# Kernel tuning notes

Hardware: AMD Instinct MI355X
Metric: run time of the kernel (lower is better)

## Reference

```python
import jax, jax.numpy as jnp
import numpy as np

B, T, DM = 2, 512, 1024
H, DH = 16, 64          # n_heads, d_head = d_model // n_heads
D, R = 32, 4            # d_manifold, metric_net rank
TEMP_MIN = 0.5


def _rope_tables(t_len, d_head):
    inv_freq = 1.0 / (10000.0 ** (jnp.arange(0, d_head, 2, dtype=jnp.float32) / d_head))
    t = jnp.arange(t_len, dtype=jnp.float32)
    freqs = t[:, None] * inv_freq[None, :]          # [T, d_head//2]
    emb = jnp.concatenate([freqs, freqs], axis=-1)  # [T, d_head]
    return jnp.cos(emb), jnp.sin(emb)


def _apply_rope(x, cos, sin):
    # x: [B, H, T, d_head]
    half = x.shape[-1] // 2
    x1, x2 = x[..., :half], x[..., half:]
    c1 = cos[None, None, :, :half]
    s1 = sin[None, None, :, :half]
    return jnp.concatenate([x1 * c1 - x2 * s1, x1 * s1 + x2 * c1], axis=-1)


def setup_inputs() -> dict:
    key = jax.random.key(0)
    ks = jax.random.split(key, 9)
    s = 0.02
    return {
        "x": jax.random.normal(ks[0], (B, T, DM), dtype=jnp.float32),
        "Wq": s * jax.random.normal(ks[1], (DM, DM), dtype=jnp.float32),
        "Wk": s * jax.random.normal(ks[2], (DM, DM), dtype=jnp.float32),
        "Wv": s * jax.random.normal(ks[3], (DM, DM), dtype=jnp.float32),
        "Wo": s * jax.random.normal(ks[4], (DM, DM), dtype=jnp.float32),
        "Wqm": s * jax.random.normal(ks[5], (DH, D), dtype=jnp.float32),
        "Wkm": s * jax.random.normal(ks[6], (DH, D), dtype=jnp.float32),
        "Wmetric": s * jax.random.normal(ks[7], (D, D * R), dtype=jnp.float32),
        "temperature": jnp.asarray(1.0, dtype=jnp.float32),
    }


def reference(x, Wq, Wk, Wv, Wo, Wqm, Wkm, Wmetric, temperature):
    b, t, c = x.shape
    # projections -> [B, H, T, d_head]
    def split_heads(y):
        return y.reshape(b, t, H, DH).transpose(0, 2, 1, 3)
    q = split_heads(x @ Wq)
    k = split_heads(x @ Wk)
    v = split_heads(x @ Wv)

    cos, sin = _rope_tables(t, DH)
    q = _apply_rope(q, cos, sin)
    k = _apply_rope(k, cos, sin)

    # manifold coordinates in (0,1): [B, H, T, D]
    qm = jax.nn.sigmoid(jnp.einsum('bhtd,dm->bhtm', q, Wqm))
    km = jax.nn.sigmoid(jnp.einsum('bhtd,dm->bhtm', k, Wkm))

    # low-rank metric factor U(q): [B, H, T, D, R]
    U = jnp.einsum('bhtm,mn->bhtn', qm, Wmetric).reshape(b, H, t, D, R)

    # Euclidean part: ||q_i - k_j||^2 = |q|^2 + |k|^2 - 2 q.k  -> [B,H,T,T]
    q2 = jnp.sum(qm * qm, axis=-1)
    k2 = jnp.sum(km * km, axis=-1)
    qk = jnp.einsum('bhid,bhjd->bhij', qm, km)
    dist_euc = q2[..., :, None] + k2[..., None, :] - 2.0 * qk

    # low-rank part: ||U_i^T (q_i - k_j)||^2, factorized as U_i^T q_i - U_i^T k_j
    Uq = jnp.einsum('bhidr,bhid->bhir', U, qm)          # [B,H,T,R]
    Uk = jnp.einsum('bhidr,bhjd->bhijr', U, km)         # [B,H,T,T,R]
    dist_lr = jnp.sum((Uq[:, :, :, None, :] - Uk) ** 2, axis=-1)

    dist_sq = jnp.maximum(dist_euc + dist_lr, 0.0)

    temp = jnp.maximum(temperature, TEMP_MIN)
    attn = -dist_sq / temp

    causal = jnp.triu(jnp.ones((t, t), dtype=bool), k=1)
    attn = jnp.where(causal[None, None], -jnp.inf, attn)
    attn = jax.nn.softmax(attn, axis=-1)

    out = jnp.einsum('bhij,bhjd->bhid', attn, v)        # [B,H,T,d_head]
    out = out.transpose(0, 2, 1, 3).reshape(b, t, c)
    return out @ Wo
```

## Files before the change

### kernel.cpp

```cpp
#include <hip/hip_runtime.h>
#include <cmath>

constexpr int B_  = 2;
constexpr int T_  = 512;
constexpr int DM_ = 1024;
constexpr int H_  = 16;
constexpr int DH_ = 64;
constexpr int D_  = 32;
constexpr int R_  = 4;
constexpr int BH_ = B_ * H_;

typedef __bf16 bf16x8 __attribute__((ext_vector_type(8)));
typedef float  f32x4  __attribute__((ext_vector_type(4)));
typedef unsigned short u16x8 __attribute__((ext_vector_type(8)));

__device__ __forceinline__ unsigned short f2bf(float f) {
    unsigned u = __float_as_uint(f);
    return (unsigned short)((u + 0x7fffu + ((u >> 16) & 1u)) >> 16);
}
__device__ __forceinline__ float bf2f(unsigned short v) {
    return __uint_as_float((unsigned)v << 16);
}
__device__ __forceinline__ void gload16(const void* g, void* l) {
    __builtin_amdgcn_global_load_lds(
        (const __attribute__((address_space(1))) void*)g,
        (__attribute__((address_space(3))) void*)l, 16, 0, 0);
}

__global__ __launch_bounds__(256) void prep_kernel(
    const float* __restrict__ x,
    const float* __restrict__ Wq, const float* __restrict__ Wk,
    const float* __restrict__ Wv, const float* __restrict__ Wo,
    unsigned short* __restrict__ xb,
    unsigned short* __restrict__ wqb, unsigned short* __restrict__ wkb,
    unsigned short* __restrict__ wvb, unsigned short* __restrict__ wob)
{
    const int t = threadIdx.x;
    const int z = blockIdx.z;
    if (z == 4) {
        int base = (blockIdx.y * 16 + blockIdx.x) * 4096 + t * 16;
#pragma unroll
        for (int c = 0; c < 4; ++c) {
            float4 v = *(const float4*)&x[base + c * 4];
            ushort4 o = { f2bf(v.x), f2bf(v.y), f2bf(v.z), f2bf(v.w) };
            *(ushort4*)&xb[base + c * 4] = o;
        }
        return;
    }
    __shared__ __align__(16) unsigned short Ls[64][72];
    const float* W = (z == 0) ? Wq : (z == 1) ? Wk : (z == 2) ? Wv : Wo;
    unsigned short* O = (z == 0) ? wqb : (z == 1) ? wkb : (z == 2) ? wvb : wob;
    const int k0 = blockIdx.x * 64;
    const int n0 = blockIdx.y * 64;
#pragma unroll
    for (int it = 0; it < 4; ++it) {
        int r = it * 16 + (t >> 4);
        int c = (t & 15) * 4;
        float4 v4 = *(const float4*)&W[(size_t)(k0 + r) * DM_ + n0 + c];
        Ls[c + 0][r] = f2bf(v4.x); Ls[c + 1][r] = f2bf(v4.y);
        Ls[c + 2][r] = f2bf(v4.z); Ls[c + 3][r] = f2bf(v4.w);
    }
    __syncthreads();
#pragma unroll
    for (int it = 0; it < 2; ++it) {
        int nl = it * 32 + (t >> 3);
        int kc = (t & 7) * 8;
        *(u16x8*)&O[(size_t)(n0 + nl) * DM_ + k0 + kc] = *(const u16x8*)&Ls[nl][kc];
    }
}

__global__ __launch_bounds__(256) void gemm_qkv(
    const unsigned short* __restrict__ A,
    const unsigned short* __restrict__ Bt0,
    const unsigned short* __restrict__ Bt1,
    const unsigned short* __restrict__ Bt2,
    float* __restrict__ C0, float* __restrict__ C1,
    unsigned short* __restrict__ vT)
{
    __shared__ __align__(16) unsigned short As[2][64 * 64];
    __shared__ __align__(16) unsigned short Bs[2][64 * 64];
    const int tid  = threadIdx.x;
    const int lane = tid & 63;
    const int w    = tid >> 6;
    const int wm   = (w & 1) * 32;
    const int wn   = (w >> 1) * 32;
    const int l15  = lane & 15, quad = lane >> 4;

    const int wg   = (blockIdx.x & 7) * 96 + (blockIdx.x >> 3);
    const int bm   = (wg & 15) * 64;
    const int nidx = wg >> 4;
    const int n0   = nidx * 64;
    const int which = n0 >> 10;
    const int bn   = n0 & 1023;
    const unsigned short* Bt = (which == 0) ? Bt0 : (which == 1) ? Bt1 : Bt2;

    const int srow = tid >> 3, kcs = tid & 7, kcg = kcs ^ (srow & 7);
    const unsigned short* Ap0 = A  + (size_t)(bm + srow) * DM_ + kcg * 8;
    const unsigned short* Bp0 = Bt + (size_t)(bn + srow) * DM_ + kcg * 8;
    const unsigned short* Ap1 = Ap0 + 32 * DM_;
    const unsigned short* Bp1 = Bp0 + 32 * DM_;

    gload16(Ap0, &As[0][tid * 8]);
    gload16(Ap1, &As[0][tid * 8 + 2048]);
    gload16(Bp0, &Bs[0][tid * 8]);
    gload16(Bp1, &Bs[0][tid * 8 + 2048]);

    f32x4 acc[2][2] = {};
#pragma unroll
    for (int k = 0; k < 16; ++k) {
        const int cur = k & 1, nxt = cur ^ 1;
        __builtin_amdgcn_s_barrier();
        if (k + 1 < 16) {
            const int off = (k + 1) * 64;
            gload16(Ap0 + off, &As[nxt][tid * 8]);
            gload16(Ap1 + off, &As[nxt][tid * 8 + 2048]);
            gload16(Bp0 + off, &Bs[nxt][tid * 8]);
            gload16(Bp1 + off, &Bs[nxt][tid * 8 + 2048]);
            __builtin_amdgcn_s_waitcnt(0x0F74);
        } else {
            __builtin_amdgcn_s_waitcnt(0x0F70);
        }
        __builtin_amdgcn_s_barrier();

        bf16x8 af[2][2], bfr[2][2];
#pragma unroll
        for (int ki = 0; ki < 2; ++ki)
#pragma unroll
            for (int i = 0; i < 2; ++i) {
                int ra = wm + i * 16 + l15;
                int rb = wn + i * 16 + l15;
                int kch = ki * 4 + quad;
                af[ki][i]  = *(const bf16x8*)&As[cur][ra * 64 + (kch ^ (ra & 7)) * 8];
                bfr[ki][i] = *(const bf16x8*)&Bs[cur][rb * 64 + (kch ^ (rb & 7)) * 8];
            }
#pragma unroll
        for (int mi = 0; mi < 2; ++mi)
#pragma unroll
            for (int ni = 0; ni < 2; ++ni) {
                acc[mi][ni] = __builtin_amdgcn_mfma_f32_16x16x32_bf16(
                    af[0][mi], bfr[0][ni], acc[mi][ni], 0, 0, 0);
                acc[mi][ni] = __builtin_amdgcn_mfma_f32_16x16x32_bf16(
                    af[1][mi], bfr[1][ni], acc[mi][ni], 0, 0, 0);
            }
    }

#pragma unroll
    for (int mi = 0; mi < 2; ++mi)
#pragma unroll
        for (int ni = 0; ni < 2; ++ni) {
            f32x4 a = acc[mi][ni];
            int col = wn + ni * 16 + l15;
            int h = bn >> 6, d = col;
#pragma unroll
            for (int r = 0; r < 4; ++r) {
                int row = bm + wm + mi * 16 + quad * 4 + r;
                int bb = row >> 9, tt = row & (T_ - 1);
                if (which == 2) {
                    vT[(((size_t)bb * H_ + h) * DH_ + d) * T_ + tt] = f2bf(a[r]);
                } else {
                    float* C = (which == 0) ? C0 : C1;
                    C[(((size_t)bb * H_ + h) * T_ + tt) * DH_ + d] = a[r];
                }
            }
        }
}

__global__ __launch_bounds__(256) void gemm_out(
    const unsigned short* __restrict__ A,
    const unsigned short* __restrict__ Bt,
    float* __restrict__ C0)
{
    __shared__ __align__(16) unsigned short As[2][64 * 64];
    __shared__ __align__(16) unsigned short Bs[2][64 * 64];
    const int tid  = threadIdx.x;
    const int lane = tid & 63;
    const int w    = tid >> 6;
    const int wm   = (w & 1) * 32;
    const int wn   = (w >> 1) * 32;
    const int l15  = lane & 15, quad = lane >> 4;

    const int bm = blockIdx.y * 64;
    const int bn = blockIdx.x * 64;

    const int srow = tid >> 3, kcs = tid & 7, kcg = kcs ^ (srow & 7);
    const unsigned short* Ap0 = A  + (size_t)(bm + srow) * DM_ + kcg * 8;
    const unsigned short* Bp0 = Bt + (size_t)(bn + srow) * DM_ + kcg * 8;
    const unsigned short* Ap1 = Ap0 + 32 * DM_;
    const unsigned short* Bp1 = Bp0 + 32 * DM_;

    gload16(Ap0, &As[0][tid * 8]);
    gload16(Ap1, &As[0][tid * 8 + 2048]);
    gload16(Bp0, &Bs[0][tid * 8]);
    gload16(Bp1, &Bs[0][tid * 8 + 2048]);

    f32x4 acc[2][2] = {};
#pragma unroll
    for (int k = 0; k < 16; ++k) {
        const int cur = k & 1, nxt = cur ^ 1;
        __builtin_amdgcn_s_barrier();
        if (k + 1 < 16) {
            const int off = (k + 1) * 64;
            gload16(Ap0 + off, &As[nxt][tid * 8]);
            gload16(Ap1 + off, &As[nxt][tid * 8 + 2048]);
            gload16(Bp0 + off, &Bs[nxt][tid * 8]);
            gload16(Bp1 + off, &Bs[nxt][tid * 8 + 2048]);
            __builtin_amdgcn_s_waitcnt(0x0F74);
        } else {
            __builtin_amdgcn_s_waitcnt(0x0F70);
        }
        __builtin_amdgcn_s_barrier();

        bf16x8 af[2][2], bfr[2][2];
#pragma unroll
        for (int ki = 0; ki < 2; ++ki)
#pragma unroll
            for (int i = 0; i < 2; ++i) {
                int ra = wm + i * 16 + l15;
                int rb = wn + i * 16 + l15;
                int kch = ki * 4 + quad;
                af[ki][i]  = *(const bf16x8*)&As[cur][ra * 64 + (kch ^ (ra & 7)) * 8];
                bfr[ki][i] = *(const bf16x8*)&Bs[cur][rb * 64 + (kch ^ (rb & 7)) * 8];
            }
#pragma unroll
        for (int mi = 0; mi < 2; ++mi)
#pragma unroll
            for (int ni = 0; ni < 2; ++ni) {
                acc[mi][ni] = __builtin_amdgcn_mfma_f32_16x16x32_bf16(
                    af[0][mi], bfr[0][ni], acc[mi][ni], 0, 0, 0);
                acc[mi][ni] = __builtin_amdgcn_mfma_f32_16x16x32_bf16(
                    af[1][mi], bfr[1][ni], acc[mi][ni], 0, 0, 0);
            }
    }

#pragma unroll
    for (int mi = 0; mi < 2; ++mi)
#pragma unroll
        for (int ni = 0; ni < 2; ++ni) {
            f32x4 a = acc[mi][ni];
            int col = wn + ni * 16 + l15;
#pragma unroll
            for (int r = 0; r < 4; ++r) {
                int row = bm + wm + mi * 16 + quad * 4 + r;
                C0[(size_t)row * DM_ + bn + col] = a[r];
            }
        }
}

__global__ __launch_bounds__(256) void feat_both(
    const float* __restrict__ q_raw, const float* __restrict__ k_raw,
    const float* __restrict__ Wqm,   const float* __restrict__ Wkm,
    const float* __restrict__ Wmetric,
    unsigned short* __restrict__ a_hi, unsigned short* __restrict__ a_lo,
    unsigned short* __restrict__ km_hi, unsigned short* __restrict__ km_lo,
    float* __restrict__ q2p, float* __restrict__ k2,
    unsigned short* __restrict__ Urb)
{
    const bool QSIDE = (blockIdx.y == 0);
    const float* raw = QSIDE ? q_raw : k_raw;
    const float* Wm  = QSIDE ? Wqm   : Wkm;

    __shared__ float qrs[4][64];
    __shared__ float qms[4][32];
    const int tid  = threadIdx.x;
    const int w    = tid >> 6;
    const int lane = tid & 63;
    const int row  = blockIdx.x * 4 + w;
    const int t    = row & (T_ - 1);
    const int bh   = row >> 9;

    const int m  = lane & 31;
    const int hh = lane >> 5;

    float rv = raw[(size_t)row * 64 + lane];
    float ang = (float)t * expf((float)m * -0.28782313662425575f);
    float s, c;
    sincosf(ang, &s, &c);
    float partner = __shfl_xor(rv, 32);
    float qr = (lane < 32) ? (rv * c - partner * s) : (partner * s + rv * c);
    qrs[w][lane] = qr;

    float acc = 0.f;
#pragma unroll 8
    for (int i = 0; i < 32; ++i) {
        int d = hh * 32 + i;
        acc += qrs[w][d] * Wm[d * 32 + m];
    }
    acc += __shfl_xor(acc, 32);
    const float qm = 1.0f / (1.0f + __expf(-acc));
    if (hh == 0) qms[w][m] = qm;

    if (!QSIDE) {
        if (lane < 32) {
            unsigned short hi = f2bf(qm);
            unsigned short lo = f2bf(qm - bf2f(hi));
            size_t off = (size_t)row * 32 + lane;
            km_hi[off] = hi; km_lo[off] = lo;
        }
        float sq = (lane < 32) ? qm * qm : 0.f;
        sq += __shfl_xor(sq, 32); sq += __shfl_xor(sq, 16);
        sq += __shfl_xor(sq, 8);  sq += __shfl_xor(sq, 4);
        sq += __shfl_xor(sq, 2);  sq += __shfl_xor(sq, 1);
        if (lane == 0) k2[row] = sq;
        return;
    }

    float a0 = 0.f, a1 = 0.f;
#pragma unroll 8
    for (int mm = 0; mm < 32; ++mm) {
        float qv = qms[w][mm];
        float2 wv = *(const float2*)&Wmetric[mm * 128 + lane * 2];
        a0 += qv * wv.x;
        a1 += qv * wv.y;
    }

    {
        int n0i = lane * 2;
        int r0 = n0i & 3, d0 = n0i >> 2;
        Urb[(((size_t)bh * R_ + r0    ) * T_ + t) * D_ + d0] = f2bf(a0);
        Urb[(((size_t)bh * R_ + r0 + 1) * T_ + t) * D_ + d0] = f2bf(a1);
    }

    float dq = qms[w][lane >> 1];
    float u0 = a0 * dq, u1 = a1 * dq;
    u0 += __shfl_xor(u0, 2);  u1 += __shfl_xor(u1, 2);
    u0 += __shfl_xor(u0, 4);  u1 += __shfl_xor(u1, 4);
    u0 += __shfl_xor(u0, 8);  u1 += __shfl_xor(u1, 8);
    u0 += __shfl_xor(u0, 16); u1 += __shfl_xor(u1, 16);
    u0 += __shfl_xor(u0, 32); u1 += __shfl_xor(u1, 32);
    float v0 = __shfl_xor(u0, 1), v1 = __shfl_xor(u1, 1);
    const bool odd = (lane & 1);
    float Uq0 = odd ? v0 : u0;
    float Uq1 = odd ? v1 : u1;
    float Uq2 = odd ? u0 : v0;
    float Uq3 = odd ? u1 : v1;

    {
        int src = m * 2;
        float s0 = __shfl(a0, src);
        float s1 = __shfl(a1, src);
        float s2 = __shfl(a0, src + 1);
        float s3 = __shfl(a1, src + 1);
        if (lane < 32) {
            float b = Uq0 * s0 + Uq1 * s1 + Uq2 * s2 + Uq3 * s3;
            float a = qm + b;
            unsigned short hi = f2bf(a);
            unsigned short lo = f2bf(a - bf2f(hi));
            size_t off = (size_t)row * 32 + lane;
            a_hi[off] = hi; a_lo[off] = lo;
        }
    }

    float sq = (lane < 32) ? qm * qm : 0.f;
    sq += __shfl_xor(sq, 32); sq += __shfl_xor(sq, 16);
    sq += __shfl_xor(sq, 8);  sq += __shfl_xor(sq, 4);
    sq += __shfl_xor(sq, 2);  sq += __shfl_xor(sq, 1);
    if (lane == 0)
        q2p[row] = sq + Uq0 * Uq0 + Uq1 * Uq1 + Uq2 * Uq2 + Uq3 * Uq3;
}

constexpr int PROW = 40;
__global__ __launch_bounds__(256) void attn_mfma(
    const unsigned short* __restrict__ a_hi, const unsigned short* __restrict__ a_lo,
    const unsigned short* __restrict__ km_hi, const unsigned short* __restrict__ km_lo,
    const unsigned short* __restrict__ Urb,
    const float* __restrict__ q2p, const float* __restrict__ k2,
    const float* __restrict__ temp_p, const unsigned short* __restrict__ vT,
    unsigned short* __restrict__ ctxb)
{
    __shared__ __align__(16) unsigned short P_lds[4][32 * PROW];
    __shared__ __align__(16) float OP[4][32][64];
    __shared__ float ML[4][32];

    const int itile = blockIdx.x, bh = blockIdx.y;
    const int i0 = itile * 32;
    const int tid = threadIdx.x, w = tid >> 6, lane = tid & 63;
    const int l15 = lane & 15, quad = lane >> 4;

    const float inv_temp = 1.0f / fmaxf(temp_p[0], 0.5f);

    bf16x8 Ahi[2], Alo[2], Aur[4][2];
#pragma unroll
    for (int mi = 0; mi < 2; ++mi) {
        size_t ab = ((size_t)bh * T_ + i0 + mi * 16 + l15) * 32 + quad * 8;
        Ahi[mi] = *(const bf16x8*)&a_hi[ab];
        Alo[mi] = *(const bf16x8*)&a_lo[ab];
#pragma unroll
        for (int r = 0; r < 4; ++r)
            Aur[r][mi] = *(const bf16x8*)
                &Urb[(((size_t)bh * R_ + r) * T_ + i0 + mi * 16 + l15) * 32 + quad * 8];
    }
    float q2r[2][4];
#pragma unroll
    for (int mi = 0; mi < 2; ++mi)
#pragma unroll
        for (int rg = 0; rg < 4; ++rg)
            q2r[mi][rg] = q2p[(size_t)bh * T_ + i0 + mi * 16 + quad * 4 + rg];

    f32x4 Oacc[2][4] = {};
    float psum[2][4] = {};

    for (int jt = w; jt <= itile; jt += 4) {
        const int j0 = jt * 32;
        bf16x8 Bhi[2], Blo[2];
#pragma unroll
        for (int ni = 0; ni < 2; ++ni) {
            size_t kb = ((size_t)bh * T_ + j0 + ni * 16 + l15) * 32 + quad * 8;
            Bhi[ni] = *(const bf16x8*)&km_hi[kb];
            Blo[ni] = *(const bf16x8*)&km_lo[kb];
        }
        f32x4 acc[2][2] = {};
#pragma unroll
        for (int mi = 0; mi < 2; ++mi)
#pragma unroll
            for (int ni = 0; ni < 2; ++ni) {
                acc[mi][ni] = __builtin_amdgcn_mfma_f32_16x16x32_bf16(
                    Alo[mi], Bhi[ni], acc[mi][ni], 0, 0, 0);
                acc[mi][ni] = __builtin_amdgcn_mfma_f32_16x16x32_bf16(
                    Ahi[mi], Blo[ni], acc[mi][ni], 0, 0, 0);
                acc[mi][ni] = __builtin_amdgcn_mfma_f32_16x16x32_bf16(
                    Ahi[mi], Bhi[ni], acc[mi][ni], 0, 0, 0);
            }
        f32x4 sq[2][2] = {};
#pragma unroll
        for (int r = 0; r < 4; ++r) {
            f32x4 ar[2][2] = {};
#pragma unroll
            for (int mi = 0; mi < 2; ++mi)
#pragma unroll
                for (int ni = 0; ni < 2; ++ni)
                    ar[mi][ni] = __builtin_amdgcn_mfma_f32_16x16x32_bf16(
                        Aur[r][mi], Bhi[ni], ar[mi][ni], 0, 0, 0);
#pragma unroll
            for (int mi = 0; mi < 2; ++mi)
#pragma unroll
                for (int ni = 0; ni < 2; ++ni)
                    sq[mi][ni] += ar[mi][ni] * ar[mi][ni];
        }
        float k2c[2];
#pragma unroll
        for (int ni = 0; ni < 2; ++ni)
            k2c[ni] = k2[(size_t)bh * T_ + j0 + ni * 16 + l15];
        const bool diag = (jt == itile);
#pragma unroll
        for (int mi = 0; mi < 2; ++mi)
#pragma unroll
            for (int ni = 0; ni < 2; ++ni)
#pragma unroll
                for (int rg = 0; rg < 4; ++rg) {
                    float dist = q2r[mi][rg] + k2c[ni]
                               - 2.f * acc[mi][ni][rg] + sq[mi][ni][rg];
                    float sc = -fmaxf(dist, 0.f) * inv_temp;
                    if (diag && (ni * 16 + l15) > (mi * 16 + quad * 4 + rg))
                        sc = -1e30f;
                    float p = __expf(sc);
                    psum[mi][rg] += p;
                    P_lds[w][(mi * 16 + quad * 4 + rg) * PROW + ni * 16 + l15] = f2bf(p);
                }
        bf16x8 Pf[2], Vf[4];
#pragma unroll
        for (int mi = 0; mi < 2; ++mi)
            Pf[mi] = *(const bf16x8*)&P_lds[w][(mi * 16 + l15) * PROW + quad * 8];
#pragma unroll
        for (int n4 = 0; n4 < 4; ++n4)
            Vf[n4] = *(const bf16x8*)
                &vT[((size_t)bh * DH_ + n4 * 16 + l15) * T_ + j0 + quad * 8];
#pragma unroll
        for (int mi = 0; mi < 2; ++mi)
#pragma unroll
            for (int n4 = 0; n4 < 4; ++n4)
                Oacc[mi][n4] = __builtin_amdgcn_mfma_f32_16x16x32_bf16(
                    Pf[mi], Vf[n4], Oacc[mi][n4], 0, 0, 0);
    }

#pragma unroll
    for (int mi = 0; mi < 2; ++mi)
#pragma unroll
        for (int rg = 0; rg < 4; ++rg) {
            float v = psum[mi][rg];
            v += __shfl_xor(v, 1); v += __shfl_xor(v, 2);
            v += __shfl_xor(v, 4); v += __shfl_xor(v, 8);
            psum[mi][rg] = v;
        }
    if (l15 == 0)
#pragma unroll
        for (int mi = 0; mi < 2; ++mi)
#pragma unroll
            for (int rg = 0; rg < 4; ++rg)
                ML[w][mi * 16 + quad * 4 + rg] = psum[mi][rg];
#pragma unroll
    for (int mi = 0; mi < 2; ++mi)
#pragma unroll
        for (int n4 = 0; n4 < 4; ++n4)
#pragma unroll
            for (int rg = 0; rg < 4; ++rg)
                OP[w][mi * 16 + quad * 4 + rg][n4 * 16 + l15] = Oacc[mi][n4][rg];
    __syncthreads();

    const int ii = tid >> 3, ds = tid & 7;
    float l = ML[0][ii] + ML[1][ii] + ML[2][ii] + ML[3][ii];
    float O[8] = {};
#pragma unroll
    for (int wv = 0; wv < 4; ++wv) {
        float4 o0 = *(const float4*)&OP[wv][ii][ds * 8];
        float4 o1 = *(const float4*)&OP[wv][ii][ds * 8 + 4];
        O[0] += o0.x; O[1] += o0.y; O[2] += o0.z; O[3] += o0.w;
        O[4] += o1.x; O[5] += o1.y; O[6] += o1.z; O[7] += o1.w;
    }
    const float inv = 1.0f / l;
    const int b = bh >> 4, h = bh & 15;
    u16x8 o;
#pragma unroll
    for (int dd = 0; dd < 8; ++dd) o[dd] = f2bf(O[dd] * inv);
    *(u16x8*)&ctxb[((size_t)b * T_ + i0 + ii) * DM_ + h * 64 + ds * 8] = o;
}

extern "C" void kernel_launch(void* const* d_in, const int* in_sizes, int n_in,
                              void* d_out, int out_size, void* d_ws, size_t ws_size,
                              hipStream_t stream)
{
    const float* x       = (const float*)d_in[0];
    const float* Wq      = (const float*)d_in[1];
    const float* Wk      = (const float*)d_in[2];
    const float* Wv      = (const float*)d_in[3];
    const float* Wo      = (const float*)d_in[4];
    const float* Wqm     = (const float*)d_in[5];
    const float* Wkm     = (const float*)d_in[6];
    const float* Wmetric = (const float*)d_in[7];
    const float* temp    = (const float*)d_in[8];
    float* out = (float*)d_out;
    float* ws  = (float*)d_ws;

    float* q_raw = ws;
    float* k_raw = q_raw + (size_t)BH_ * T_ * DH_;
    float* q2p   = k_raw + (size_t)BH_ * T_ * DH_;
    float* k2    = q2p   + (size_t)BH_ * T_;
    unsigned short* xb   = (unsigned short*)(k2 + (size_t)BH_ * T_);
    unsigned short* wqb  = xb   + (size_t)DM_ * DM_;
    unsigned short* wkb  = wqb  + (size_t)DM_ * DM_;
    unsigned short* wvb  = wkb  + (size_t)DM_ * DM_;
    unsigned short* wob  = wvb  + (size_t)DM_ * DM_;
    unsigned short* a_hi = wob  + (size_t)DM_ * DM_;
    unsigned short* a_lo = a_hi + (size_t)BH_ * T_ * D_;
    unsigned short* kmhi = a_lo + (size_t)BH_ * T_ * D_;
    unsigned short* kmlo = kmhi + (size_t)BH_ * T_ * D_;
    unsigned short* Urb  = kmlo + (size_t)BH_ * T_ * D_;
    unsigned short* vT   = Urb  + (size_t)BH_ * R_ * T_ * D_;
    unsigned short* ctxb = (unsigned short*)q_raw;

    prep_kernel<<<dim3(16, 16, 5), 256, 0, stream>>>(
        x, Wq, Wk, Wv, Wo, xb, wqb, wkb, wvb, wob);
    gemm_qkv<<<dim3(768), 256, 0, stream>>>(
        xb, wqb, wkb, wvb, q_raw, k_raw, vT);
    feat_both<<<dim3(BH_ * T_ / 4, 2), 256, 0, stream>>>(
        q_raw, k_raw, Wqm, Wkm, Wmetric,
        a_hi, a_lo, kmhi, kmlo, q2p, k2, Urb);
    attn_mfma<<<dim3(T_ / 32, BH_), 256, 0, stream>>>(
        a_hi, a_lo, kmhi, kmlo, Urb, q2p, k2, temp, vT, ctxb);
    gemm_out<<<dim3(16, 16), 256, 0, stream>>>(
        ctxb, wob, out);
}
```

Before: 149.5 us.

## Fuse all stages into one persistent kernel with software grid barriers

Replaces the five separate kernel launches (weight/input bf16 conversion, QKV GEMM, feature computation, attention, output GEMM) with one persistent kernel of 512 blocks. The stages run as grid-stride loops separated by an atomic-counter grid barrier, and a memset resets the counter before launch. The goal is to remove launch gaps and tail effects between the small stages. In exchange, every stage gets the same 512-block grid and shared-memory budget, the spin barriers cost time, and correctness depends on all 512 blocks being co-resident.

After: 363.4 us. 143% more time.

```diff
diff --git a/kernel.cpp b/kernel.cpp
--- a/kernel.cpp
+++ b/kernel.cpp
@@ -27,491 +27,489 @@
         (__attribute__((address_space(3))) void*)l, 16, 0, 0);
 }
 
-__global__ __launch_bounds__(256) void prep_kernel(
-    const float* __restrict__ x,
-    const float* __restrict__ Wq, const float* __restrict__ Wk,
-    const float* __restrict__ Wv, const float* __restrict__ Wo,
-    unsigned short* __restrict__ xb,
-    unsigned short* __restrict__ wqb, unsigned short* __restrict__ wkb,
-    unsigned short* __restrict__ wvb, unsigned short* __restrict__ wob)
-{
-    const int t = threadIdx.x;
-    const int z = blockIdx.z;
-    if (z == 4) {
-        int base = (blockIdx.y * 16 + blockIdx.x) * 4096 + t * 16;
-#pragma unroll
-        for (int c = 0; c < 4; ++c) {
-            float4 v = *(const float4*)&x[base + c * 4];
-            ushort4 o = { f2bf(v.x), f2bf(v.y), f2bf(v.z), f2bf(v.w) };
-            *(ushort4*)&xb[base + c * 4] = o;
-        }
-        return;
-    }
-    __shared__ __align__(16) unsigned short Ls[64][72];
-    const float* W = (z == 0) ? Wq : (z == 1) ? Wk : (z == 2) ? Wv : Wo;
-    unsigned short* O = (z == 0) ? wqb : (z == 1) ? wkb : (z == 2) ? wvb : wob;
-    const int k0 = blockIdx.x * 64;
-    const int n0 = blockIdx.y * 64;
-#pragma unroll
-    for (int it = 0; it < 4; ++it) {
-        int r = it * 16 + (t >> 4);
-        int c = (t & 15) * 4;
-        float4 v4 = *(const float4*)&W[(size_t)(k0 + r) * DM_ + n0 + c];
-        Ls[c + 0][r] = f2bf(v4.x); Ls[c + 1][r] = f2bf(v4.y);
-        Ls[c + 2][r] = f2bf(v4.z); Ls[c + 3][r] = f2bf(v4.w);
+constexpr int PROW = 40;
+
+__device__ __forceinline__ void grid_barrier(unsigned* cnt, unsigned target) {
+    __syncthreads();
+    if (threadIdx.x == 0) {
+        __threadfence();
+        atomicAdd(cnt, 1u);
+        while (atomicAdd(cnt, 0u) < target)
+            __builtin_amdgcn_s_sleep(8);
+        __threadfence();
     }
     __syncthreads();
-#pragma unroll
-    for (int it = 0; it < 2; ++it) {
-        int nl = it * 32 + (t >> 3);
-        int kc = (t & 7) * 8;
-        *(u16x8*)&O[(size_t)(n0 + nl) * DM_ + k0 + kc] = *(const u16x8*)&Ls[nl][kc];
-    }
 }
 
-__global__ __launch_bounds__(256) void gemm_qkv(
-    const unsigned short* __restrict__ A,
-    const unsigned short* __restrict__ Bt0,
-    const unsigned short* __restrict__ Bt1,
-    const unsigned short* __restrict__ Bt2,
-    float* __restrict__ C0, float* __restrict__ C1,
-    unsigned short* __restrict__ vT)
+__global__ __launch_bounds__(256, 2) void mega(
+    const float* x, const float* Wq, const float* Wk,
+    const float* Wv, const float* Wo,
+    const float* Wqm, const float* Wkm, const float* Wmetric,
+    const float* temp_p, float* out,
+    unsigned short* xb, unsigned short* wqb, unsigned short* wkb,
+    unsigned short* wvb, unsigned short* wob,
+    float* q_raw, float* k_raw, float* q2p, float* k2,
+    unsigned short* a_hi, unsigned short* a_lo,
+    unsigned short* km_hi, unsigned short* km_lo,
+    unsigned short* Urb, unsigned short* vT, unsigned short* ctxb,
+    unsigned* bar)
 {
-    __shared__ __align__(16) unsigned short As[2][64 * 64];
-    __shared__ __align__(16) unsigned short Bs[2][64 * 64];
+    __shared__ __align__(16) unsigned char smem[45056];
+
     const int tid  = threadIdx.x;
     const int lane = tid & 63;
     const int w    = tid >> 6;
-    const int wm   = (w & 1) * 32;
-    const int wn   = (w >> 1) * 32;
     const int l15  = lane & 15, quad = lane >> 4;
 
-    const int wg   = (blockIdx.x & 7) * 96 + (blockIdx.x >> 3);
-    const int bm   = (wg & 15) * 64;
-    const int nidx = wg >> 4;
-    const int n0   = nidx * 64;
-    const int which = n0 >> 10;
-    const int bn   = n0 & 1023;
-    const unsigned short* Bt = (which == 0) ? Bt0 : (which == 1) ? Bt1 : Bt2;
-
-    const int srow = tid >> 3, kcs = tid & 7, kcg = kcs ^ (srow & 7);
-    const unsigned short* Ap0 = A  + (size_t)(bm + srow) * DM_ + kcg * 8;
-    const unsigned short* Bp0 = Bt + (size_t)(bn + srow) * DM_ + kcg * 8;
-    const unsigned short* Ap1 = Ap0 + 32 * DM_;
-    const unsigned short* Bp1 = Bp0 + 32 * DM_;
-
-    gload16(Ap0, &As[0][tid * 8]);
-    gload16(Ap1, &As[0][tid * 8 + 2048]);
-    gload16(Bp0, &Bs[0][tid * 8]);
-    gload16(Bp1, &Bs[0][tid * 8 + 2048]);
-
-    f32x4 acc[2][2] = {};
-#pragma unroll
-    for (int k = 0; k < 16; ++k) {
-        const int cur = k & 1, nxt = cur ^ 1;
-        __builtin_amdgcn_s_barrier();
-        if (k + 1 < 16) {
-            const int off = (k + 1) * 64;
-            gload16(Ap0 + off, &As[nxt][tid * 8]);
-            gload16(Ap1 + off, &As[nxt][tid * 8 + 2048]);
-            gload16(Bp0 + off, &Bs[nxt][tid * 8]);
-            gload16(Bp1 + off, &Bs[nxt][tid * 8 + 2048]);
-            __builtin_amdgcn_s_waitcnt(0x0F74);
-        } else {
-            __builtin_amdgcn_s_waitcnt(0x0F70);
-        }
-        __builtin_amdgcn_s_barrier();
-
-        bf16x8 af[2][2], bfr[2][2];
-#pragma unroll
-        for (int ki = 0; ki < 2; ++ki)
-#pragma unroll
-            for (int i = 0; i < 2; ++i) {
-                int ra = wm + i * 16 + l15;
-                int rb = wn + i * 16 + l15;
-                int kch = ki * 4 + quad;
-                af[ki][i]  = *(const bf16x8*)&As[cur][ra * 64 + (kch ^ (ra & 7)) * 8];
-                bfr[ki][i] = *(const bf16x8*)&Bs[cur][rb * 64 + (kch ^ (rb & 7)) * 8];
-            }
+    {
+        unsigned short (*Ls)[72] = (unsigned short(*)[72])smem;
+        for (int u = blockIdx.x; u < 1280; u += gridDim.x) {
+            const int z  = u >> 8;
+            const int ux = u & 15;
+            const int uy = (u >> 4) & 15;
+            if (z == 4) {
+                int base = (uy * 16 + ux) * 4096 + tid * 16;
+#pragma unroll
+                for (int c = 0; c < 4; ++c) {
+                    float4 v = *(const float4*)&x[base + c * 4];
+                    ushort4 o = { f2bf(v.x), f2bf(v.y), f2bf(v.z), f2bf(v.w) };
+                    *(ushort4*)&xb[base + c * 4] = o;
+                }
+            } else {
+                const float* W = (z == 0) ? Wq : (z == 1) ? Wk : (z == 2) ? Wv : Wo;
+                unsigned short* O = (z == 0) ? wqb : (z == 1) ? wkb : (z == 2) ? wvb : wob;
+                const int k0 = ux * 64;
+                const int n0 = uy * 64;
+#pragma unroll
+                for (int it = 0; it < 4; ++it) {
+                    int r = it * 16 + (tid >> 4);
+                    int c = (tid & 15) * 4;
+                    float4 v4 = *(const float4*)&W[(size_t)(k0 + r) * DM_ + n0 + c];
+                    Ls[c + 0][r] = f2bf(v4.x); Ls[c + 1][r] = f2bf(v4.y);
+                    Ls[c + 2][r] = f2bf(v4.z); Ls[c + 3][r] = f2bf(v4.w);
+                }
+                __syncthreads();
+#pragma unroll
+                for (int it = 0; it < 2; ++it) {
+                    int nl = it * 32 + (tid >> 3);
+                    int kc = (tid & 7) * 8;
+                    *(u16x8*)&O[(size_t)(n0 + nl) * DM_ + k0 + kc] = *(const u16x8*)&Ls[nl][kc];
+                }
+                __syncthreads();
+            }
+        }
+    }
+    grid_barrier(bar, 1u * gridDim.x);
+
+    {
+        unsigned short* As0 = (unsigned short*)smem;
+        unsigned short* Bs0 = (unsigned short*)(smem + 16384);
+        const int wm = (w & 1) * 32;
+        const int wn = (w >> 1) * 32;
+        const int srow = tid >> 3, kcs = tid & 7, kcg = kcs ^ (srow & 7);
+
+        for (int u = blockIdx.x; u < 768; u += gridDim.x) {
+            const int bm = (u / 48) * 64;
+            const int n0 = (u % 48) * 64;
+            const int which = n0 >> 10;
+            const int bn = n0 & 1023;
+            const unsigned short* Bt = (which == 0) ? wqb : (which == 1) ? wkb : wvb;
+
+            const unsigned short* Ap0 = xb + (size_t)(bm + srow) * DM_ + kcg * 8;
+            const unsigned short* Bp0 = Bt + (size_t)(bn + srow) * DM_ + kcg * 8;
+            const unsigned short* Ap1 = Ap0 + 32 * DM_;
+            const unsigned short* Bp1 = Bp0 + 32 * DM_;
+
+            gload16(Ap0, &As0[tid * 8]);
+            gload16(Ap1, &As0[tid * 8 + 2048]);
+            gload16(Bp0, &Bs0[tid * 8]);
+            gload16(Bp1, &Bs0[tid * 8 + 2048]);
+
+            f32x4 acc[2][2] = {};
+#pragma unroll
+            for (int k = 0; k < 16; ++k) {
+                const int cur = k & 1, nxt = cur ^ 1;
+                __builtin_amdgcn_s_barrier();
+                if (k + 1 < 16) {
+                    const int off = (k + 1) * 64;
+                    gload16(Ap0 + off, &As0[nxt * 4096 + tid * 8]);
+                    gload16(Ap1 + off, &As0[nxt * 4096 + tid * 8 + 2048]);
+                    gload16(Bp0 + off, &Bs0[nxt * 4096 + tid * 8]);
+                    gload16(Bp1 + off, &Bs0[nxt * 4096 + tid * 8 + 2048]);
+                    __builtin_amdgcn_s_waitcnt(0x0F74);
+                } else {
+                    __builtin_amdgcn_s_waitcnt(0x0F70);
+                }
+                __builtin_amdgcn_s_barrier();
+
+                bf16x8 af[2][2], bfr[2][2];
+#pragma unroll
+                for (int ki = 0; ki < 2; ++ki)
+#pragma unroll
+                    for (int i = 0; i < 2; ++i) {
+                        int ra = wm + i * 16 + l15;
+                        int rb = wn + i * 16 + l15;
+                        int kch = ki * 4 + quad;
+                        af[ki][i]  = *(const bf16x8*)&As0[cur * 4096 + ra * 64 + (kch ^ (ra & 7)) * 8];
+                        bfr[ki][i] = *(const bf16x8*)&Bs0[cur * 4096 + rb * 64 + (kch ^ (rb & 7)) * 8];
+                    }
+#pragma unroll
+                for (int mi = 0; mi < 2; ++mi)
+#pragma unroll
+                    for (int ni = 0; ni < 2; ++ni) {
+                        acc[mi][ni] = __builtin_amdgcn_mfma_f32_16x16x32_bf16(
+                            af[0][mi], bfr[0][ni], acc[mi][ni], 0, 0, 0);
+                        acc[mi][ni] = __builtin_amdgcn_mfma_f32_16x16x32_bf16(
+                            af[1][mi], bfr[1][ni], acc[mi][ni], 0, 0, 0);
+                    }
+            }
+
+#pragma unroll
+            for (int mi = 0; mi < 2; ++mi)
+#pragma unroll
+                for (int ni = 0; ni < 2; ++ni) {
+                    f32x4 a = acc[mi][ni];
+                    int col = wn + ni * 16 + l15;
+                    int h = bn >> 6, d = col;
+#pragma unroll
+                    for (int r = 0; r < 4; ++r) {
+                        int row = bm + wm + mi * 16 + quad * 4 + r;
+                        int bb = row >> 9, tt = row & (T_ - 1);
+                        if (which == 2) {
+                            vT[(((size_t)bb * H_ + h) * DH_ + d) * T_ + tt] = f2bf(a[r]);
+                        } else {
+                            float* C = (which == 0) ? q_raw : k_raw;
+                            C[(((size_t)bb * H_ + h) * T_ + tt) * DH_ + d] = a[r];
+                        }
+                    }
+                }
+        }
+    }
+    grid_barrier(bar, 2u * gridDim.x);
+
+    {
+        float* fs  = (float*)smem;
+        float* qrs = fs + w * 96;
+        float* qms = qrs + 64;
+        const int m  = lane & 31;
+        const int hh = lane >> 5;
+        const int gwave = blockIdx.x * 4 + w;
+
+        for (int u = gwave; u < 32768; u += 2048) {
+            const bool QSIDE = (u < 16384);
+            const int row = u & 16383;
+            const float* raw = QSIDE ? q_raw : k_raw;
+            const float* Wm  = QSIDE ? Wqm   : Wkm;
+            const int t  = row & (T_ - 1);
+            const int bh = row >> 9;
+
+            float rv = raw[(size_t)row * 64 + lane];
+            float ang = (float)t * expf((float)m * -0.28782313662425575f);
+            float s, c;
+            sincosf(ang, &s, &c);
+            float partner = __shfl_xor(rv, 32);
+            float qr = (lane < 32) ? (rv * c - partner * s) : (partner * s + rv * c);
+            qrs[lane] = qr;
+
+            float acc = 0.f;
+#pragma unroll 8
+            for (int i = 0; i < 32; ++i) {
+                int d = hh * 32 + i;
+                acc += qrs[d] * Wm[d * 32 + m];
+            }
+            acc += __shfl_xor(acc, 32);
+            const float qm = 1.0f / (1.0f + __expf(-acc));
+            if (hh == 0) qms[m] = qm;
+
+            if (!QSIDE) {
+                if (lane < 32) {
+                    unsigned short hi = f2bf(qm);
+                    unsigned short lo = f2bf(qm - bf2f(hi));
+                    size_t off = (size_t)row * 32 + lane;
+                    km_hi[off] = hi; km_lo[off] = lo;
+                }
+                float sq = (lane < 32) ? qm * qm : 0.f;
+                sq += __shfl_xor(sq, 32); sq += __shfl_xor(sq, 16);
+                sq += __shfl_xor(sq, 8);  sq += __shfl_xor(sq, 4);
+                sq += __shfl_xor(sq, 2);  sq += __shfl_xor(sq, 1);
+                if (lane == 0) k2[row] = sq;
+                continue;
+            }
+
+            float a0 = 0.f, a1 = 0.f;
+#pragma unroll 8
+            for (int mm = 0; mm < 32; ++mm) {
+                float qv = qms[mm];
+                float2 wv = *(const float2*)&Wmetric[mm * 128 + lane * 2];
+                a0 += qv * wv.x;
+                a1 += qv * wv.y;
+            }
+            {
+                int n0i = lane * 2;
+                int r0 = n0i & 3, d0 = n0i >> 2;
+                Urb[(((size_t)bh * R_ + r0    ) * T_ + t) * D_ + d0] = f2bf(a0);
+                Urb[(((size_t)bh * R_ + r0 + 1) * T_ + t) * D_ + d0] = f2bf(a1);
+            }
+
+            float dq = qms[lane >> 1];
+            float u0 = a0 * dq, u1 = a1 * dq;
+            u0 += __shfl_xor(u0, 2);  u1 += __shfl_xor(u1, 2);
+            u0 += __shfl_xor(u0, 4);  u1 += __shfl_xor(u1, 4);
+            u0 += __shfl_xor(u0, 8);  u1 += __shfl_xor(u1, 8);
+            u0 += __shfl_xor(u0, 16); u1 += __shfl_xor(u1, 16);
+            u0 += __shfl_xor(u0, 32); u1 += __shfl_xor(u1, 32);
+            float v0 = __shfl_xor(u0, 1), v1 = __shfl_xor(u1, 1);
+            const bool odd = (lane & 1);
+            float Uq0 = odd ? v0 : u0;
+            float Uq1 = odd ? v1 : u1;
+            float Uq2 = odd ? u0 : v0;
+            float Uq3 = odd ? u1 : v1;
+
+            {
+                int src = m * 2;
+                float s0 = __shfl(a0, src);
+                float s1 = __shfl(a1, src);
+                float s2 = __shfl(a0, src + 1);
+                float s3 = __shfl(a1, src + 1);
+                if (lane < 32) {
+                    float b = Uq0 * s0 + Uq1 * s1 + Uq2 * s2 + Uq3 * s3;
+                    float a = qm + b;
+                    unsigned short hi = f2bf(a);
+                    unsigned short lo = f2bf(a - bf2f(hi));
+                    size_t off = (size_t)row * 32 + lane;
+                    a_hi[off] = hi; a_lo[off] = lo;
+                }
+            }
+
+            float sq = (lane < 32) ? qm * qm : 0.f;
+            sq += __shfl_xor(sq, 32); sq += __shfl_xor(sq, 16);
+            sq += __shfl_xor(sq, 8);  sq += __shfl_xor(sq, 4);
+            sq += __shfl_xor(sq, 2);  sq += __shfl_xor(sq, 1);
+            if (lane == 0)
+                q2p[row] = sq + Uq0 * Uq0 + Uq1 * Uq1 + Uq2 * Uq2 + Uq3 * Uq3;
+        }
+    }
+    grid_barrier(bar, 3u * gridDim.x);
+
+    {
+        unsigned short* P  = (unsigned short*)smem;
+        float* OPf = (float*)(smem + 10240);
+        float* MLf = (float*)(smem + 43008);
+
+        const int u = blockIdx.x;
+        const int itile = u & 15, bh = u >> 4;
+        const int i0 = itile * 32;
+        const float inv_temp = 1.0f / fmaxf(temp_p[0], 0.5f);
+
+        bf16x8 Ahi[2], Alo[2], Aur[4][2];
+#pragma unroll
+        for (int mi = 0; mi < 2; ++mi) {
+            size_t ab = ((size_t)bh * T_ + i0 + mi * 16 + l15) * 32 + quad * 8;
+            Ahi[mi] = *(const bf16x8*)&a_hi[ab];
+            Alo[mi] = *(const bf16x8*)&a_lo[ab];
+#pragma unroll
+            for (int r = 0; r < 4; ++r)
+                Aur[r][mi] = *(const bf16x8*)
+                    &Urb[(((size_t)bh * R_ + r) * T_ + i0 + mi * 16 + l15) * 32 + quad * 8];
+        }
+        float q2r[2][4];
 #pragma unroll
         for (int mi = 0; mi < 2; ++mi)
 #pragma unroll
+            for (int rg = 0; rg < 4; ++rg)
+                q2r[mi][rg] = q2p[(size_t)bh * T_ + i0 + mi * 16 + quad * 4 + rg];
+
+        f32x4 Oacc[2][4] = {};
+        float psum[2][4] = {};
+
+        for (int jt = w; jt <= itile; jt += 4) {
+            const int j0 = jt * 32;
+            bf16x8 Bhi[2], Blo[2];
+#pragma unroll
             for (int ni = 0; ni < 2; ++ni) {
-                acc[mi][ni] = __builtin_amdgcn_mfma_f32_16x16x32_bf16(
-                    af[0][mi], bfr[0][ni], acc[mi][ni], 0, 0, 0);
-                acc[mi][ni] = __builtin_amdgcn_mfma_f32_16x16x32_bf16(
-                    af[1][mi], bfr[1][ni], acc[mi][ni], 0, 0, 0);
-            }
+                size_t kb = ((size_t)bh * T_ + j0 + ni * 16 + l15) * 32 + quad * 8;
+                Bhi[ni] = *(const bf16x8*)&km_hi[kb];
+                Blo[ni] = *(const bf16x8*)&km_lo[kb];
+            }
+            f32x4 acc[2][2] = {};
+#pragma unroll
+            for (int mi = 0; mi < 2; ++mi)
+#pragma unroll
+                for (int ni = 0; ni < 2; ++ni) {
+                    acc[mi][ni] = __builtin_amdgcn_mfma_f32_16x16x32_bf16(
+                        Alo[mi], Bhi[ni], acc[mi][ni], 0, 0, 0);
+                    acc[mi][ni] = __builtin_amdgcn_mfma_f32_16x16x32_bf16(
+                        Ahi[mi], Blo[ni], acc[mi][ni], 0, 0, 0);
+                    acc[mi][ni] = __builtin_amdgcn_mfma_f32_16x16x32_bf16(
+                        Ahi[mi], Bhi[ni], acc[mi][ni], 0, 0, 0);
+                }
+            f32x4 sq[2][2] = {};
+#pragma unroll
+            for (int r = 0; r < 4; ++r) {
+                f32x4 ar[2][2] = {};
+#pragma unroll
+                for (int mi = 0; mi < 2; ++mi)
+#pragma unroll
+                    for (int ni = 0; ni < 2; ++ni)
+                        ar[mi][ni] = __builtin_amdgcn_mfma_f32_16x16x32_bf16(
+                            Aur[r][mi], Bhi[ni], ar[mi][ni], 0, 0, 0);
+#pragma unroll
+                for (int mi = 0; mi < 2; ++mi)
+#pragma unroll
+                    for (int ni = 0; ni < 2; ++ni)
+                        sq[mi][ni] += ar[mi][ni] * ar[mi][ni];
+            }
+            float k2c[2];
+#pragma unroll
+            for (int ni = 0; ni < 2; ++ni)
+                k2c[ni] = k2[(size_t)bh * T_ + j0 + ni * 16 + l15];
+            const bool diag = (jt == itile);
+#pragma unroll
+            for (int mi = 0; mi < 2; ++mi)
+#pragma unroll
+                for (int ni = 0; ni < 2; ++ni)
+#pragma unroll
+                    for (int rg = 0; rg < 4; ++rg) {
+                        float dist = q2r[mi][rg] + k2c[ni]
+                                   - 2.f * acc[mi][ni][rg] + sq[mi][ni][rg];
+                        float sc = -fmaxf(dist, 0.f) * inv_temp;
+                        if (diag && (ni * 16 + l15) > (mi * 16 + quad * 4 + rg))
+                            sc = -1e30f;
+                        float p = __expf(sc);
+                        psum[mi][rg] += p;
+                        P[w * 1280 + (mi * 16 + quad * 4 + rg) * PROW + ni * 16 + l15] = f2bf(p);
+                    }
+            bf16x8 Pf[2], Vf[4];
+#pragma unroll
+            for (int mi = 0; mi < 2; ++mi)
+                Pf[mi] = *(const bf16x8*)&P[w * 1280 + (mi * 16 + l15) * PROW + quad * 8];
+#pragma unroll
+            for (int n4 = 0; n4 < 4; ++n4)
+                Vf[n4] = *(const bf16x8*)
+                    &vT[((size_t)bh * DH_ + n4 * 16 + l15) * T_ + j0 + quad * 8];
+#pragma unroll
+            for (int mi = 0; mi < 2; ++mi)
+#pragma unroll
+                for (int n4 = 0; n4 < 4; ++n4)
+                    Oacc[mi][n4] = __builtin_amdgcn_mfma_f32_16x16x32_bf16(
+                        Pf[mi], Vf[n4], Oacc[mi][n4], 0, 0, 0);
+        }
+
+#pragma unroll
+        for (int mi = 0; mi < 2; ++mi)
+#pragma unroll
+            for (int rg = 0; rg < 4; ++rg) {
+                float v = psum[mi][rg];
+                v += __shfl_xor(v, 1); v += __shfl_xor(v, 2);
+                v += __shfl_xor(v, 4); v += __shfl_xor(v, 8);
+                psum[mi][rg] = v;
+            }
+        if (l15 == 0)
+#pragma unroll
+            for (int mi = 0; mi < 2; ++mi)
+#pragma unroll
+                for (int rg = 0; rg < 4; ++rg)
+                    MLf[w * 32 + mi * 16 + quad * 4 + rg] = psum[mi][rg];
+#pragma unroll
+        for (int mi = 0; mi < 2; ++mi)
+#pragma unroll
+            for (int n4 = 0; n4 < 4; ++n4)
+#pragma unroll
+                for (int rg = 0; rg < 4; ++rg)
+                    OPf[(w * 32 + mi * 16 + quad * 4 + rg) * 64 + n4 * 16 + l15] = Oacc[mi][n4][rg];
+        __syncthreads();
+
+        const int ii = tid >> 3, ds = tid & 7;
+        float l = MLf[0 * 32 + ii] + MLf[1 * 32 + ii] + MLf[2 * 32 + ii] + MLf[3 * 32 + ii];
+        float O[8] = {};
+#pragma unroll
+        for (int wv = 0; wv < 4; ++wv) {
+            float4 o0 = *(const float4*)&OPf[(wv * 32 + ii) * 64 + ds * 8];
+            float4 o1 = *(const float4*)&OPf[(wv * 32 + ii) * 64 + ds * 8 + 4];
+            O[0] += o0.x; O[1] += o0.y; O[2] += o0.z; O[3] += o0.w;
+            O[4] += o1.x; O[5] += o1.y; O[6] += o1.z; O[7] += o1.w;
+        }
+        const float inv = 1.0f / l;
+        const int b = bh >> 4, h = bh & 15;
+        u16x8 o;
+#pragma unroll
+        for (int dd = 0; dd < 8; ++dd) o[dd] = f2bf(O[dd] * inv);
+        *(u16x8*)&ctxb[((size_t)b * T_ + i0 + ii) * DM_ + h * 64 + ds * 8] = o;
     }
-
-#pragma unroll
-    for (int mi = 0; mi < 2; ++mi)
-#pragma unroll
-        for (int ni = 0; ni < 2; ++ni) {
-            f32x4 a = acc[mi][ni];
-            int col = wn + ni * 16 + l15;
-            int h = bn >> 6, d = col;
-#pragma unroll
-            for (int r = 0; r < 4; ++r) {
-                int row = bm + wm + mi * 16 + quad * 4 + r;
-                int bb = row >> 9, tt = row & (T_ - 1);
-                if (which == 2) {
-                    vT[(((size_t)bb * H_ + h) * DH_ + d) * T_ + tt] = f2bf(a[r]);
-                } else {
-                    float* C = (which == 0) ? C0 : C1;
-                    C[(((size_t)bb * H_ + h) * T_ + tt) * DH_ + d] = a[r];
-                }
-            }
-        }
-}
-
-__global__ __launch_bounds__(256) void gemm_out(
-    const unsigned short* __restrict__ A,
-    const unsigned short* __restrict__ Bt,
-    float* __restrict__ C0)
-{
-    __shared__ __align__(16) unsigned short As[2][64 * 64];
-    __shared__ __align__(16) unsigned short Bs[2][64 * 64];
-    const int tid  = threadIdx.x;
-    const int lane = tid & 63;
-    const int w    = tid >> 6;
-    const int wm   = (w & 1) * 32;
-    const int wn   = (w >> 1) * 32;
-    const int l15  = lane & 15, quad = lane >> 4;
-
-    const int bm = blockIdx.y * 64;
-    const int bn = blockIdx.x * 64;
-
-    const int srow = tid >> 3, kcs = tid & 7, kcg = kcs ^ (srow & 7);
-    const unsigned short* Ap0 = A  + (size_t)(bm + srow) * DM_ + kcg * 8;
-    const unsigned short* Bp0 = Bt + (size_t)(bn + srow) * DM_ + kcg * 8;
-    const unsigned short* Ap1 = Ap0 + 32 * DM_;
-    const unsigned short* Bp1 = Bp0 + 32 * DM_;
-
-    gload16(Ap0, &As[0][tid * 8]);
-    gload16(Ap1, &As[0][tid * 8 + 2048]);
-    gload16(Bp0, &Bs[0][tid * 8]);
-    gload16(Bp1, &Bs[0][tid * 8 + 2048]);
-
-    f32x4 acc[2][2] = {};
-#pragma unroll
-    for (int k = 0; k < 16; ++k) {
-        const int cur = k & 1, nxt = cur ^ 1;
-        __builtin_amdgcn_s_barrier();
-        if (k + 1 < 16) {
-            const int off = (k + 1) * 64;
-            gload16(Ap0 + off, &As[nxt][tid * 8]);
-            gload16(Ap1 + off, &As[nxt][tid * 8 + 2048]);
-            gload16(Bp0 + off, &Bs[nxt][tid * 8]);
-            gload16(Bp1 + off, &Bs[nxt][tid * 8 + 2048]);
-            __builtin_amdgcn_s_waitcnt(0x0F74);
-        } else {
-            __builtin_amdgcn_s_waitcnt(0x0F70);
-        }
-        __builtin_amdgcn_s_barrier();
-
-        bf16x8 af[2][2], bfr[2][2];
-#pragma unroll
-        for (int ki = 0; ki < 2; ++ki)
-#pragma unroll
-            for (int i = 0; i < 2; ++i) {
-                int ra = wm + i * 16 + l15;
-                int rb = wn + i * 16 + l15;
-                int kch = ki * 4 + quad;
-                af[ki][i]  = *(const bf16x8*)&As[cur][ra * 64 + (kch ^ (ra & 7)) * 8];
-                bfr[ki][i] = *(const bf16x8*)&Bs[cur][rb * 64 + (kch ^ (rb & 7)) * 8];
-            }
+    grid_barrier(bar, 4u * gridDim.x);
+
+    if (blockIdx.x < 256) {
+        unsigned short* As0 = (unsigned short*)smem;
+        unsigned short* Bs0 = (unsigned short*)(smem + 16384);
+        const int wm = (w & 1) * 32;
+        const int wn = (w >> 1) * 32;
+        const int srow = tid >> 3, kcs = tid & 7, kcg = kcs ^ (srow & 7);
+
+        const int bm = (blockIdx.x >> 4) * 64;
+        const int bn = (blockIdx.x & 15) * 64;
+
+        const unsigned short* Ap0 = ctxb + (size_t)(bm + srow) * DM_ + kcg * 8;
+        const unsigned short* Bp0 = wob  + (size_t)(bn + srow) * DM_ + kcg * 8;
+        const unsigned short* Ap1 = Ap0 + 32 * DM_;
+        const unsigned short* Bp1 = Bp0 + 32 * DM_;
+
+        gload16(Ap0, &As0[tid * 8]);
+        gload16(Ap1, &As0[tid * 8 + 2048]);
+        gload16(Bp0, &Bs0[tid * 8]);
+        gload16(Bp1, &Bs0[tid * 8 + 2048]);
+
+        f32x4 acc[2][2] = {};
+#pragma unroll
+        for (int k = 0; k < 16; ++k) {
+            const int cur = k & 1, nxt = cur ^ 1;
+            __builtin_amdgcn_s_barrier();
+            if (k + 1 < 16) {
+                const int off = (k + 1) * 64;
+                gload16(Ap0 + off, &As0[nxt * 4096 + tid * 8]);
+                gload16(Ap1 + off, &As0[nxt * 4096 + tid * 8 + 2048]);
+                gload16(Bp0 + off, &Bs0[nxt * 4096 + tid * 8]);
+                gload16(Bp1 + off, &Bs0[nxt * 4096 + tid * 8 + 2048]);
+                __builtin_amdgcn_s_waitcnt(0x0F74);
+            } else {
+                __builtin_amdgcn_s_waitcnt(0x0F70);
+            }
+            __builtin_amdgcn_s_barrier();
+
+            bf16x8 af[2][2], bfr[2][2];
+#pragma unroll
+            for (int ki = 0; ki < 2; ++ki)
+#pragma unroll
+                for (int i = 0; i < 2; ++i) {
+                    int ra = wm + i * 16 + l15;
+                    int rb = wn + i * 16 + l15;
+                    int kch = ki * 4 + quad;
+                    af[ki][i]  = *(const bf16x8*)&As0[cur * 4096 + ra * 64 + (kch ^ (ra & 7)) * 8];
+                    bfr[ki][i] = *(const bf16x8*)&Bs0[cur * 4096 + rb * 64 + (kch ^ (rb & 7)) * 8];
+                }
+#pragma unroll
+            for (int mi = 0; mi < 2; ++mi)
+#pragma unroll
+                for (int ni = 0; ni < 2; ++ni) {
+                    acc[mi][ni] = __builtin_amdgcn_mfma_f32_16x16x32_bf16(
+                        af[0][mi], bfr[0][ni], acc[mi][ni], 0, 0, 0);
+                    acc[mi][ni] = __builtin_amdgcn_mfma_f32_16x16x32_bf16(
+                        af[1][mi], bfr[1][ni], acc[mi][ni], 0, 0, 0);
+                }
+        }
+
 #pragma unroll
         for (int mi = 0; mi < 2; ++mi)
 #pragma unroll
             for (int ni = 0; ni < 2; ++ni) {
-                acc[mi][ni] = __builtin_amdgcn_mfma_f32_16x16x32_bf16(
-                    af[0][mi], bfr[0][ni], acc[mi][ni], 0, 0, 0);
-                acc[mi][ni] = __builtin_amdgcn_mfma_f32_16x16x32_bf16(
-                    af[1][mi], bfr[1][ni], acc[mi][ni], 0, 0, 0);
+                f32x4 a = acc[mi][ni];
+                int col = wn + ni * 16 + l15;
+#pragma unroll
+                for (int r = 0; r < 4; ++r) {
+                    int row = bm + wm + mi * 16 + quad * 4 + r;
+                    out[(size_t)row * DM_ + bn + col] = a[r];
+                }
             }
     }
-
-#pragma unroll
-    for (int mi = 0; mi < 2; ++mi)
-#pragma unroll
-        for (int ni = 0; ni < 2; ++ni) {
-            f32x4 a = acc[mi][ni];
-            int col = wn + ni * 16 + l15;
-#pragma unroll
-            for (int r = 0; r < 4; ++r) {
-                int row = bm + wm + mi * 16 + quad * 4 + r;
-                C0[(size_t)row * DM_ + bn + col] = a[r];
-            }
-        }
-}
-
-__global__ __launch_bounds__(256) void feat_both(
-    const float* __restrict__ q_raw, const float* __restrict__ k_raw,
-    const float* __restrict__ Wqm,   const float* __restrict__ Wkm,
-    const float* __restrict__ Wmetric,
-    unsigned short* __restrict__ a_hi, unsigned short* __restrict__ a_lo,
-    unsigned short* __restrict__ km_hi, unsigned short* __restrict__ km_lo,
-    float* __restrict__ q2p, float* __restrict__ k2,
-    unsigned short* __restrict__ Urb)
-{
-    const bool QSIDE = (blockIdx.y == 0);
-    const float* raw = QSIDE ? q_raw : k_raw;
-    const float* Wm  = QSIDE ? Wqm   : Wkm;
-
-    __shared__ float qrs[4][64];
-    __shared__ float qms[4][32];
-    const int tid  = threadIdx.x;
-    const int w    = tid >> 6;
-    const int lane = tid & 63;
-    const int row  = blockIdx.x * 4 + w;
-    const int t    = row & (T_ - 1);
-    const int bh   = row >> 9;
-
-    const int m  = lane & 31;
-    const int hh = lane >> 5;
-
-    float rv = raw[(size_t)row * 64 + lane];
-    float ang = (float)t * expf((float)m * -0.28782313662425575f);
-    float s, c;
-    sincosf(ang, &s, &c);
-    float partner = __shfl_xor(rv, 32);
-    float qr = (lane < 32) ? (rv * c - partner * s) : (partner * s + rv * c);
-    qrs[w][lane] = qr;
-
-    float acc = 0.f;
-#pragma unroll 8
-    for (int i = 0; i < 32; ++i) {
-        int d = hh * 32 + i;
-        acc += qrs[w][d] * Wm[d * 32 + m];
-    }
-    acc += __shfl_xor(acc, 32);
-    const float qm = 1.0f / (1.0f + __expf(-acc));
-    if (hh == 0) qms[w][m] = qm;
-
-    if (!QSIDE) {
-        if (lane < 32) {
-            unsigned short hi = f2bf(qm);
-            unsigned short lo = f2bf(qm - bf2f(hi));
-            size_t off = (size_t)row * 32 + lane;
-            km_hi[off] = hi; km_lo[off] = lo;
-        }
-        float sq = (lane < 32) ? qm * qm : 0.f;
-        sq += __shfl_xor(sq, 32); sq += __shfl_xor(sq, 16);
-        sq += __shfl_xor(sq, 8);  sq += __shfl_xor(sq, 4);
-        sq += __shfl_xor(sq, 2);  sq += __shfl_xor(sq, 1);
-        if (lane == 0) k2[row] = sq;
-        return;
-    }
-
-    float a0 = 0.f, a1 = 0.f;
-#pragma unroll 8
-    for (int mm = 0; mm < 32; ++mm) {
-        float qv = qms[w][mm];
-        float2 wv = *(const float2*)&Wmetric[mm * 128 + lane * 2];
-        a0 += qv * wv.x;
-        a1 += qv * wv.y;
-    }
-
-    {
-        int n0i = lane * 2;
-        int r0 = n0i & 3, d0 = n0i >> 2;
-        Urb[(((size_t)bh * R_ + r0    ) * T_ + t) * D_ + d0] = f2bf(a0);
-        Urb[(((size_t)bh * R_ + r0 + 1) * T_ + t) * D_ + d0] = f2bf(a1);
-    }
-
-    float dq = qms[w][lane >> 1];
-    float u0 = a0 * dq, u1 = a1 * dq;
-    u0 += __shfl_xor(u0, 2);  u1 += __shfl_xor(u1, 2);
-    u0 += __shfl_xor(u0, 4);  u1 += __shfl_xor(u1, 4);
-    u0 += __shfl_xor(u0, 8);  u1 += __shfl_xor(u1, 8);
-    u0 += __shfl_xor(u0, 16); u1 += __shfl_xor(u1, 16);
-    u0 += __shfl_xor(u0, 32); u1 += __shfl_xor(u1, 32);
-    float v0 = __shfl_xor(u0, 1), v1 = __shfl_xor(u1, 1);
-    const bool odd = (lane & 1);
-    float Uq0 = odd ? v0 : u0;
-    float Uq1 = odd ? v1 : u1;
-    float Uq2 = odd ? u0 : v0;
-    float Uq3 = odd ? u1 : v1;
-
-    {
-        int src = m * 2;
-        float s0 = __shfl(a0, src);
-        float s1 = __shfl(a1, src);
-        float s2 = __shfl(a0, src + 1);
-        float s3 = __shfl(a1, src + 1);
-        if (lane < 32) {
-            float b = Uq0 * s0 + Uq1 * s1 + Uq2 * s2 + Uq3 * s3;
-            float a = qm + b;
-            unsigned short hi = f2bf(a);
-            unsigned short lo = f2bf(a - bf2f(hi));
-            size_t off = (size_t)row * 32 + lane;
-            a_hi[off] = hi; a_lo[off] = lo;
-        }
-    }
-
-    float sq = (lane < 32) ? qm * qm : 0.f;
-    sq += __shfl_xor(sq, 32); sq += __shfl_xor(sq, 16);
-    sq += __shfl_xor(sq, 8);  sq += __shfl_xor(sq, 4);
-    sq += __shfl_xor(sq, 2);  sq += __shfl_xor(sq, 1);
-    if (lane == 0)
-        q2p[row] = sq + Uq0 * Uq0 + Uq1 * Uq1 + Uq2 * Uq2 + Uq3 * Uq3;
-}
-
-constexpr int PROW = 40;
-__global__ __launch_bounds__(256) void attn_mfma(
-    const unsigned short* __restrict__ a_hi, const unsigned short* __restrict__ a_lo,
-    const unsigned short* __restrict__ km_hi, const unsigned short* __restrict__ km_lo,
-    const unsigned short* __restrict__ Urb,
-    const float* __restrict__ q2p, const float* __restrict__ k2,
-    const float* __restrict__ temp_p, const unsigned short* __restrict__ vT,
-    unsigned short* __restrict__ ctxb)
-{
-    __shared__ __align__(16) unsigned short P_lds[4][32 * PROW];
-    __shared__ __align__(16) float OP[4][32][64];
-    __shared__ float ML[4][32];
-
-    const int itile = blockIdx.x, bh = blockIdx.y;
-    const int i0 = itile * 32;
-    const int tid = threadIdx.x, w = tid >> 6, lane = tid & 63;
-    const int l15 = lane & 15, quad = lane >> 4;
-
-    const float inv_temp = 1.0f / fmaxf(temp_p[0], 0.5f);
-
-    bf16x8 Ahi[2], Alo[2], Aur[4][2];
-#pragma unroll
-    for (int mi = 0; mi < 2; ++mi) {
-        size_t ab = ((size_t)bh * T_ + i0 + mi * 16 + l15) * 32 + quad * 8;
-        Ahi[mi] = *(const bf16x8*)&a_hi[ab];
-        Alo[mi] = *(const bf16x8*)&a_lo[ab];
-#pragma unroll
-        for (int r = 0; r < 4; ++r)
-            Aur[r][mi] = *(const bf16x8*)
-                &Urb[(((size_t)bh * R_ + r) * T_ + i0 + mi * 16 + l15) * 32 + quad * 8];
-    }
-    float q2r[2][4];
-#pragma unroll
-    for (int mi = 0; mi < 2; ++mi)
-#pragma unroll
-        for (int rg = 0; rg < 4; ++rg)
-            q2r[mi][rg] = q2p[(size_t)bh * T_ + i0 + mi * 16 + quad * 4 + rg];
-
-    f32x4 Oacc[2][4] = {};
-    float psum[2][4] = {};
-
-    for (int jt = w; jt <= itile; jt += 4) {
-        const int j0 = jt * 32;
-        bf16x8 Bhi[2], Blo[2];
-#pragma unroll
-        for (int ni = 0; ni < 2; ++ni) {
-            size_t kb = ((size_t)bh * T_ + j0 + ni * 16 + l15) * 32 + quad * 8;
-            Bhi[ni] = *(const bf16x8*)&km_hi[kb];
-            Blo[ni] = *(const bf16x8*)&km_lo[kb];
-        }
-        f32x4 acc[2][2] = {};
-#pragma unroll
-        for (int mi = 0; mi < 2; ++mi)
-#pragma unroll
-            for (int ni = 0; ni < 2; ++ni) {
-                acc[mi][ni] = __builtin_amdgcn_mfma_f32_16x16x32_bf16(
-                    Alo[mi], Bhi[ni], acc[mi][ni], 0, 0, 0);
-                acc[mi][ni] = __builtin_amdgcn_mfma_f32_16x16x32_bf16(
-                    Ahi[mi], Blo[ni], acc[mi][ni], 0, 0, 0);
-                acc[mi][ni] = __builtin_amdgcn_mfma_f32_16x16x32_bf16(
-                    Ahi[mi], Bhi[ni], acc[mi][ni], 0, 0, 0);
-            }
-        f32x4 sq[2][2] = {};
-#pragma unroll
-        for (int r = 0; r < 4; ++r) {
-            f32x4 ar[2][2] = {};
-#pragma unroll
-            for (int mi = 0; mi < 2; ++mi)
-#pragma unroll
-                for (int ni = 0; ni < 2; ++ni)
-                    ar[mi][ni] = __builtin_amdgcn_mfma_f32_16x16x32_bf16(
-                        Aur[r][mi], Bhi[ni], ar[mi][ni], 0, 0, 0);
-#pragma unroll
-            for (int mi = 0; mi < 2; ++mi)
-#pragma unroll
-                for (int ni = 0; ni < 2; ++ni)
-                    sq[mi][ni] += ar[mi][ni] * ar[mi][ni];
-        }
-        float k2c[2];
-#pragma unroll
-        for (int ni = 0; ni < 2; ++ni)
-            k2c[ni] = k2[(size_t)bh * T_ + j0 + ni * 16 + l15];
-        const bool diag = (jt == itile);
-#pragma unroll
-        for (int mi = 0; mi < 2; ++mi)
-#pragma unroll
-            for (int ni = 0; ni < 2; ++ni)
-#pragma unroll
-                for (int rg = 0; rg < 4; ++rg) {
-                    float dist = q2r[mi][rg] + k2c[ni]
-                               - 2.f * acc[mi][ni][rg] + sq[mi][ni][rg];
-                    float sc = -fmaxf(dist, 0.f) * inv_temp;
-                    if (diag && (ni * 16 + l15) > (mi * 16 + quad * 4 + rg))
-                        sc = -1e30f;
-                    float p = __expf(sc);
-                    psum[mi][rg] += p;
-                    P_lds[w][(mi * 16 + quad * 4 + rg) * PROW + ni * 16 + l15] = f2bf(p);
-                }
-        bf16x8 Pf[2], Vf[4];
-#pragma unroll
-        for (int mi = 0; mi < 2; ++mi)
-            Pf[mi] = *(const bf16x8*)&P_lds[w][(mi * 16 + l15) * PROW + quad * 8];
-#pragma unroll
-        for (int n4 = 0; n4 < 4; ++n4)
-            Vf[n4] = *(const bf16x8*)
-                &vT[((size_t)bh * DH_ + n4 * 16 + l15) * T_ + j0 + quad * 8];
-#pragma unroll
-        for (int mi = 0; mi < 2; ++mi)
-#pragma unroll
-            for (int n4 = 0; n4 < 4; ++n4)
-                Oacc[mi][n4] = __builtin_amdgcn_mfma_f32_16x16x32_bf16(
-                    Pf[mi], Vf[n4], Oacc[mi][n4], 0, 0, 0);
-    }
-
-#pragma unroll
-    for (int mi = 0; mi < 2; ++mi)
-#pragma unroll
-        for (int rg = 0; rg < 4; ++rg) {
-            float v = psum[mi][rg];
-            v += __shfl_xor(v, 1); v += __shfl_xor(v, 2);
-            v += __shfl_xor(v, 4); v += __shfl_xor(v, 8);
-            psum[mi][rg] = v;
-        }
-    if (l15 == 0)
-#pragma unroll
-        for (int mi = 0; mi < 2; ++mi)
-#pragma unroll
-            for (int rg = 0; rg < 4; ++rg)
-                ML[w][mi * 16 + quad * 4 + rg] = psum[mi][rg];
-#pragma unroll
-    for (int mi = 0; mi < 2; ++mi)
-#pragma unroll
-        for (int n4 = 0; n4 < 4; ++n4)
-#pragma unroll
-            for (int rg = 0; rg < 4; ++rg)
-                OP[w][mi * 16 + quad * 4 + rg][n4 * 16 + l15] = Oacc[mi][n4][rg];
-    __syncthreads();
-
-    const int ii = tid >> 3, ds = tid & 7;
-    float l = ML[0][ii] + ML[1][ii] + ML[2][ii] + ML[3][ii];
-    float O[8] = {};
-#pragma unroll
-    for (int wv = 0; wv < 4; ++wv) {
-        float4 o0 = *(const float4*)&OP[wv][ii][ds * 8];
-        float4 o1 = *(const float4*)&OP[wv][ii][ds * 8 + 4];
-        O[0] += o0.x; O[1] += o0.y; O[2] += o0.z; O[3] += o0.w;
-        O[4] += o1.x; O[5] += o1.y; O[6] += o1.z; O[7] += o1.w;
-    }
-    const float inv = 1.0f / l;
-    const int b = bh >> 4, h = bh & 15;
-    u16x8 o;
-#pragma unroll
-    for (int dd = 0; dd < 8; ++dd) o[dd] = f2bf(O[dd] * inv);
-    *(u16x8*)&ctxb[((size_t)b * T_ + i0 + ii) * DM_ + h * 64 + ds * 8] = o;
 }
 
 extern "C" void kernel_launch(void* const* d_in, const int* in_sizes, int n_in,
@@ -546,16 +544,12 @@
     unsigned short* Urb  = kmlo + (size_t)BH_ * T_ * D_;
     unsigned short* vT   = Urb  + (size_t)BH_ * R_ * T_ * D_;
     unsigned short* ctxb = (unsigned short*)q_raw;
-
-    prep_kernel<<<dim3(16, 16, 5), 256, 0, stream>>>(
-        x, Wq, Wk, Wv, Wo, xb, wqb, wkb, wvb, wob);
-    gemm_qkv<<<dim3(768), 256, 0, stream>>>(
-        xb, wqb, wkb, wvb, q_raw, k_raw, vT);
-    feat_both<<<dim3(BH_ * T_ / 4, 2), 256, 0, stream>>>(
-        q_raw, k_raw, Wqm, Wkm, Wmetric,
-        a_hi, a_lo, kmhi, kmlo, q2p, k2, Urb);
-    attn_mfma<<<dim3(T_ / 32, BH_), 256, 0, stream>>>(
-        a_hi, a_lo, kmhi, kmlo, Urb, q2p, k2, temp, vT, ctxb);
-    gemm_out<<<dim3(16, 16), 256, 0, stream>>>(
-        ctxb, wob, out);
+    unsigned* bar = (unsigned*)(vT + (size_t)BH_ * DH_ * T_);
+
+    hipMemsetAsync(bar, 0, 64, stream);
+
+    mega<<<dim3(512), dim3(256), 0, stream>>>(
+        x, Wq, Wk, Wv, Wo, Wqm, Wkm, Wmetric, temp, out,
+        xb, wqb, wkb, wvb, wob, q_raw, k_raw, q2p, k2,
+        a_hi, a_lo, kmhi, kmlo, Urb, vT, ctxb, bar);
 }
```
